# Kernel tuning notes

Hardware: AMD Instinct MI355X
Metric: run time of the kernel (lower is better)

The kernel has to match this reference:

```python
import jax, jax.numpy as jnp
import numpy as np

N_NODES = 100000
N_EDGES = 1600000
N_PAIRS = 200000
IN_C, HID_C, OUT_C = 128, 128, 64


def setup_inputs() -> dict:
    key = jax.random.key(0)
    ks = jax.random.split(key, 10)
    x = jax.random.normal(ks[0], (N_NODES, IN_C), dtype=jnp.float32)
    edge_index = jax.random.randint(ks[1], (2, N_EDGES), 0, N_NODES, dtype=jnp.int64)
    node_i = jax.random.randint(ks[2], (N_PAIRS,), 0, N_NODES, dtype=jnp.int64)
    node_j = jax.random.randint(ks[3], (N_PAIRS,), 0, N_NODES, dtype=jnp.int64)
    def glorot(k, fan_in, fan_out):
        s = jnp.sqrt(6.0 / (fan_in + fan_out))
        return jax.random.uniform(k, (fan_in, fan_out), jnp.float32, -s, s)
    W1 = glorot(ks[4], IN_C, HID_C)
    b1 = jnp.zeros((HID_C,), jnp.float32)
    W2 = glorot(ks[5], HID_C, HID_C)
    b2 = jnp.zeros((HID_C,), jnp.float32)
    W3 = glorot(ks[6], HID_C, OUT_C)
    b3 = jnp.zeros((OUT_C,), jnp.float32)
    return {"x": x, "edge_index": edge_index, "node_i": node_i, "node_j": node_j,
            "W1": W1, "b1": b1, "W2": W2, "b2": b2, "W3": W3, "b3": b3}


def _gcn_layer(h, src, dst, deg_inv, w_e, W, b):
    # h: [N, Cin] -> linear then symmetric-normalized aggregation (with self loops)
    h = h @ W  # [N, Cout]
    msg = h[src] * w_e[:, None]  # [E, Cout] gather + edge weight
    agg = jax.ops.segment_sum(msg, dst, num_segments=N_NODES)
    agg = agg + h * deg_inv[:, None]  # self-loop term: h_i / deg_i
    return agg + b


def reference(x, edge_index, node_i, node_j, W1, b1, W2, b2, W3, b3):
    src, dst = edge_index[0], edge_index[1]
    # GCN normalization with self loops: deg_i = 1 + in-degree
    ones = jnp.ones((N_EDGES,), jnp.float32)
    deg = jax.ops.segment_sum(ones, dst, num_segments=N_NODES) + 1.0
    dinv_sqrt = jax.lax.rsqrt(deg)
    deg_inv = 1.0 / deg
    w_e = dinv_sqrt[src] * dinv_sqrt[dst]  # [E]

    h = _gcn_layer(x, src, dst, deg_inv, w_e, W1, b1)
    h = jax.nn.relu(h)  # dropout is identity in eval mode
    h = _gcn_layer(h, src, dst, deg_inv, w_e, W2, b2)
    h = jax.nn.relu(h)
    h = _gcn_layer(h, src, dst, deg_inv, w_e, W3, b3)

    # dot-product link decode (decode_type=None)
    return jnp.sum(h[node_i] * h[node_j], axis=-1)  # [N_PAIRS]
```

## Files before the change

kernel.cpp:

```cpp
#include <hip/hip_runtime.h>

#define NN 100000
#define NNP 100032
#define NE 1600000
#define NP 200000
#define NBKT 782
#define BCAP 3072
#define BKB 4096

typedef short s16x8 __attribute__((ext_vector_type(8)));
typedef float f32x4 __attribute__((ext_vector_type(4)));

__device__ __forceinline__ unsigned short f2bf(float f) {
  unsigned int u = __float_as_uint(f);
  u += 0x7fffu + ((u >> 16) & 1u);
  return (unsigned short)(u >> 16);
}

__device__ __forceinline__ void upadd(uint u, float& lo, float& hi) {
  lo += __uint_as_float(u << 16);
  hi += __uint_as_float(u & 0xffff0000u);
}

template <int NT>
__device__ __forceinline__ void prepw_dev(const float* __restrict__ W,
                                          uint* __restrict__ Wt, int tid) {
  constexpr int COUT = NT * 16;
  if (tid >= 4 * NT * 64) return;
  int lane = tid & 63, comb = tid >> 6;
  int ks = comb / NT, tl = comb % NT;
  int q = lane >> 4, n = lane & 15;
  uint w[4];
#pragma unroll
  for (int jj = 0; jj < 4; ++jj) {
    int k0 = ks * 32 + q * 8 + 2 * jj;
    uint lo = f2bf(W[k0 * COUT + tl * 16 + n]);
    uint hi = f2bf(W[(k0 + 1) * COUT + tl * 16 + n]);
    w[jj] = lo | (hi << 16);
  }
  ((uint4*)Wt)[comb * 64 + lane] = make_uint4(w[0], w[1], w[2], w[3]);
}

__global__ __launch_bounds__(256) void k_setup(const float* __restrict__ W1,
                                               const float* __restrict__ W2,
                                               const float* __restrict__ W3,
                                               uint* __restrict__ Wt1,
                                               uint* __restrict__ Wt2,
                                               uint* __restrict__ Wt3,
                                               int* __restrict__ gcur) {
  int b = blockIdx.x, t = threadIdx.x;
  if (b < 4) {
    int i = b * 256 + t;
    if (i < 1024) gcur[i] = i * BCAP;
  } else if (b < 12) {
    prepw_dev<8>(W1, Wt1, (b - 4) * 256 + t);
  } else if (b < 20) {
    prepw_dev<8>(W2, Wt2, (b - 12) * 256 + t);
  } else {
    prepw_dev<4>(W3, Wt3, (b - 20) * 256 + t);
  }
}

__global__ __launch_bounds__(256) void k_bucket(const int* __restrict__ ei,
                                                int* __restrict__ gcur,
                                                int* __restrict__ aux) {
  __shared__ int cnt[1024];
  __shared__ int scn[1024];
  __shared__ int cur[1024];
  __shared__ int sc[256];
  __shared__ int sorted[BKB];
  __shared__ unsigned short sbkt[BKB];
  const int t = threadIdx.x;
  const int base = blockIdx.x * BKB;

  for (int i = t; i < 1024; i += 256) cnt[i] = 0;
  __syncthreads();

  int pk[16], bk[16];
#pragma unroll
  for (int i = 0; i < 16; ++i) {
    int e = base + t + 256 * i;
    if (e < NE) {
      int src = ei[e], dst = ei[NE + e];
      bk[i] = dst >> 7;
      pk[i] = src | ((dst & 127) << 17);
      atomicAdd(&cnt[bk[i]], 1);
    } else {
      bk[i] = -1;
    }
  }
  __syncthreads();

  int s0 = cnt[4 * t], s1 = cnt[4 * t + 1], s2 = cnt[4 * t + 2], s3 = cnt[4 * t + 3];
  int local = s0 + s1 + s2 + s3;
  sc[t] = local;
  __syncthreads();
  for (int off = 1; off < 256; off <<= 1) {
    int a = (t >= off) ? sc[t - off] : 0;
    __syncthreads();
    sc[t] += a;
    __syncthreads();
  }
  int b0 = sc[t] - local;
  scn[4 * t] = b0;
  scn[4 * t + 1] = b0 + s0;
  scn[4 * t + 2] = b0 + s0 + s1;
  scn[4 * t + 3] = b0 + s0 + s1 + s2;
  cur[4 * t] = scn[4 * t];
  cur[4 * t + 1] = scn[4 * t + 1];
  cur[4 * t + 2] = scn[4 * t + 2];
  cur[4 * t + 3] = scn[4 * t + 3];
  __syncthreads();
  const int tot = sc[255];

#pragma unroll
  for (int i = 0; i < 16; ++i) {
    if (bk[i] >= 0) {
      int pos = atomicAdd(&cur[bk[i]], 1);
      sorted[pos] = pk[i];
      sbkt[pos] = (unsigned short)bk[i];
    }
  }
  __syncthreads();

  for (int b = t; b < 1024; b += 256) {
    int c = cnt[b];
    if (c > 0) cur[b] = atomicAdd(&gcur[b], c);
  }
  __syncthreads();

  for (int k = t; k < tot; k += 256) {
    int b = sbkt[k];
    aux[cur[b] + (k - scn[b])] = sorted[k];
  }
}

__global__ __launch_bounds__(256) void k_csr(const int* __restrict__ gcur,
                                             const int* __restrict__ aux,
                                             int* __restrict__ row_ptr,
                                             float* __restrict__ dinv,
                                             int* __restrict__ col) {
  __shared__ int red[256];
  __shared__ int c[128];
  __shared__ int cur[128];
  const int b = blockIdx.x, t = threadIdx.x;
  int p = 0;
  for (int i = t; i < b; i += 256) p += gcur[i] - i * BCAP;
  red[t] = p;
  if (t < 128) c[t] = 0;
  __syncthreads();
  for (int off = 128; off > 0; off >>= 1) {
    if (t < off) red[t] += red[t + off];
    __syncthreads();
  }
  const int base = red[0];
  const int m = gcur[b] - b * BCAP;
  const int* a = aux + (size_t)b * BCAP;
  __syncthreads();
  for (int k = t; k < m; k += 256) atomicAdd(&c[a[k] >> 17], 1);
  __syncthreads();
  int val = (t < 128) ? c[t] : 0;
  red[t] = val;
  __syncthreads();
  for (int off = 1; off < 128; off <<= 1) {
    int add = (t >= off && t < 128) ? red[t - off] : 0;
    __syncthreads();
    if (t < 128) red[t] += add;
    __syncthreads();
  }
  if (t < 128) {
    int excl = red[t] - val + base;
    int node = b * 128 + t;
    if (node < NN) {
      row_ptr[node] = excl;
      dinv[node] = rsqrtf((float)(val + 1));
      cur[t] = excl;
    }
  }
  if (b == NBKT - 1 && t == 0) row_ptr[NN] = base + m;
  __syncthreads();
  for (int k = t; k < m; k += 256) {
    int pk2 = a[k];
    int pos = atomicAdd(&cur[pk2 >> 17], 1);
    col[pos] = pk2 & 0x1FFFF;
  }
}

template <int COUT, bool AFP32>
__global__ __launch_bounds__(256) void k_gemm_mfma(const void* __restrict__ Av,
                                                   const uint* __restrict__ Wt,
                                                   const float* __restrict__ dinv,
                                                   unsigned short* __restrict__ T) {
  constexpr int NT = COUT / 16;
  __shared__ __align__(16) uint Wlds[4 * NT * 64 * 4];
  __shared__ __align__(16) unsigned short Obuf[64 * COUT];
  const int t = threadIdx.x;
  {
    const uint4* src = (const uint4*)Wt;
    uint4* dst = (uint4*)Wlds;
    for (int i = t; i < 4 * NT * 64; i += 256) dst[i] = src[i];
  }
  __syncthreads();

  const int wv = t >> 6, lane = t & 63;
  const int n = lane & 15, quad = lane >> 4;
  const int rbase = blockIdx.x * 64 + wv * 16;

  union AB { uint4 u; s16x8 s; };
  AB a[4];
  if constexpr (AFP32) {
    const float* A = (const float*)Av;
    int row = rbase + n;
    if (row >= NN) row = NN - 1;
    const float* ap = A + (size_t)row * 128;
#pragma unroll
    for (int ks = 0; ks < 4; ++ks) {
      float4 v0 = *(const float4*)(ap + ks * 32 + quad * 8);
      float4 v1 = *(const float4*)(ap + ks * 32 + quad * 8 + 4);
      a[ks].u.x = (uint)f2bf(v0.x) | ((uint)f2bf(v0.y) << 16);
      a[ks].u.y = (uint)f2bf(v0.z) | ((uint)f2bf(v0.w) << 16);
      a[ks].u.z = (uint)f2bf(v1.x) | ((uint)f2bf(v1.y) << 16);
      a[ks].u.w = (uint)f2bf(v1.z) | ((uint)f2bf(v1.w) << 16);
    }
  } else {
    const uint4* A = (const uint4*)Av;
    int row = rbase + n;
#pragma unroll
    for (int ks = 0; ks < 4; ++ks) a[ks].u = A[(size_t)row * 16 + ks * 4 + quad];
  }

  f32x4 acc[NT];
#pragma unroll
  for (int tl = 0; tl < NT; ++tl) acc[tl] = (f32x4){0.f, 0.f, 0.f, 0.f};

#pragma unroll
  for (int ks = 0; ks < 4; ++ks) {
#pragma unroll
    for (int tl = 0; tl < NT; ++tl) {
      AB b;
      b.u = *(const uint4*)&Wlds[((ks * NT + tl) * 64 + lane) * 4];
      acc[tl] = __builtin_amdgcn_mfma_f32_16x16x32_bf16(a[ks].s, b.s, acc[tl], 0, 0, 0);
    }
  }

  float4 dv = *(const float4*)(dinv + rbase + quad * 4);
  float dvv[4] = {dv.x, dv.y, dv.z, dv.w};
  unsigned short* ob = Obuf + wv * 16 * COUT;
#pragma unroll
  for (int tl = 0; tl < NT; ++tl)
#pragma unroll
    for (int r = 0; r < 4; ++r)
      ob[(quad * 4 + r) * COUT + tl * 16 + n] = f2bf(acc[tl][r] * dvv[r]);

  uint4* gdst = (uint4*)(T + (size_t)rbase * COUT);
  constexpr int ITER = COUT / 32;
#pragma unroll
  for (int i = 0; i < ITER; ++i) {
    int off16 = i * 64 + lane;
    int lrow = (off16 * 8) / COUT;
    uint4 v = make_uint4(0u, 0u, 0u, 0u);
    if (rbase + lrow < NN) v = *(const uint4*)&ob[off16 * 8];
    gdst[off16] = v;
  }
}

__global__ __launch_bounds__(256) void k_gather12(const int* __restrict__ row_ptr,
                                                  const int* __restrict__ col,
                                                  const uint4* __restrict__ T4,
                                                  const float* __restrict__ dinv,
                                                  const float* __restrict__ bias,
                                                  uint4* __restrict__ An) {
  int w = (blockIdx.x * 256 + threadIdx.x) >> 6;
  int lane = threadIdx.x & 63;
  if (w >= NN) return;
  int s = row_ptr[w], tend = row_ptr[w + 1];
  const int q = lane >> 4;
  const int cl = lane & 15;
  float acc[8] = {0.f, 0.f, 0.f, 0.f, 0.f, 0.f, 0.f, 0.f};
  if (q == 0) {
    uint4 u = T4[(size_t)w * 16 + cl];
    upadd(u.x, acc[0], acc[1]);
    upadd(u.y, acc[2], acc[3]);
    upadd(u.z, acc[4], acc[5]);
    upadd(u.w, acc[6], acc[7]);
  }
  const int iters = (tend - s + 15) >> 4;
  const int m = tend - 1;
  int e = s + q;
  for (int it = 0; it < iters; ++it, e += 16) {
    int i0 = e, i1 = e + 4, i2 = e + 8, i3 = e + 12;
    int c0 = col[min(i0, m)], c1 = col[min(i1, m)];
    int c2 = col[min(i2, m)], c3 = col[min(i3, m)];
    c0 = (i0 < tend) ? c0 : NN;
    c1 = (i1 < tend) ? c1 : NN;
    c2 = (i2 < tend) ? c2 : NN;
    c3 = (i3 < tend) ? c3 : NN;
    uint4 v0 = T4[(size_t)c0 * 16 + cl];
    uint4 v1 = T4[(size_t)c1 * 16 + cl];
    uint4 v2 = T4[(size_t)c2 * 16 + cl];
    uint4 v3 = T4[(size_t)c3 * 16 + cl];
    upadd(v0.x, acc[0], acc[1]); upadd(v0.y, acc[2], acc[3]);
    upadd(v0.z, acc[4], acc[5]); upadd(v0.w, acc[6], acc[7]);
    upadd(v1.x, acc[0], acc[1]); upadd(v1.y, acc[2], acc[3]);
    upadd(v1.z, acc[4], acc[5]); upadd(v1.w, acc[6], acc[7]);
    upadd(v2.x, acc[0], acc[1]); upadd(v2.y, acc[2], acc[3]);
    upadd(v2.z, acc[4], acc[5]); upadd(v2.w, acc[6], acc[7]);
    upadd(v3.x, acc[0], acc[1]); upadd(v3.y, acc[2], acc[3]);
    upadd(v3.z, acc[4], acc[5]); upadd(v3.w, acc[6], acc[7]);
  }
#pragma unroll
  for (int i = 0; i < 8; ++i) {
    acc[i] += __shfl_down(acc[i], 16, 64);
    acc[i] += __shfl_down(acc[i], 32, 64);
  }
  if (q == 0) {
    float4 b0 = *(const float4*)&bias[cl * 8];
    float4 b1 = *(const float4*)&bias[cl * 8 + 4];
    float dv = dinv[w];
    float r[8];
    r[0] = fmaxf(fmaf(dv, acc[0], b0.x), 0.f);
    r[1] = fmaxf(fmaf(dv, acc[1], b0.y), 0.f);
    r[2] = fmaxf(fmaf(dv, acc[2], b0.z), 0.f);
    r[3] = fmaxf(fmaf(dv, acc[3], b0.w), 0.f);
    r[4] = fmaxf(fmaf(dv, acc[4], b1.x), 0.f);
    r[5] = fmaxf(fmaf(dv, acc[5], b1.y), 0.f);
    r[6] = fmaxf(fmaf(dv, acc[6], b1.z), 0.f);
    r[7] = fmaxf(fmaf(dv, acc[7], b1.w), 0.f);
    uint4 o;
    o.x = (uint)f2bf(r[0]) | ((uint)f2bf(r[1]) << 16);
    o.y = (uint)f2bf(r[2]) | ((uint)f2bf(r[3]) << 16);
    o.z = (uint)f2bf(r[4]) | ((uint)f2bf(r[5]) << 16);
    o.w = (uint)f2bf(r[6]) | ((uint)f2bf(r[7]) << 16);
    An[(size_t)w * 16 + cl] = o;
  }
}

__global__ __launch_bounds__(256) void k_gather3(const int* __restrict__ row_ptr,
                                                 const int* __restrict__ col,
                                                 const uint4* __restrict__ T4,
                                                 float* __restrict__ G3) {
  int w = (blockIdx.x * 256 + threadIdx.x) >> 6;
  int lane = threadIdx.x & 63;
  if (w >= NN) return;
  int s = row_ptr[w], tend = row_ptr[w + 1];
  const int g = lane >> 3;
  const int cl = lane & 7;
  float acc[8] = {0.f, 0.f, 0.f, 0.f, 0.f, 0.f, 0.f, 0.f};
  if (g == 0) {
    uint4 u = T4[(size_t)w * 8 + cl];
    upadd(u.x, acc[0], acc[1]);
    upadd(u.y, acc[2], acc[3]);
    upadd(u.z, acc[4], acc[5]);
    upadd(u.w, acc[6], acc[7]);
  }
  const int iters = (tend - s + 15) >> 4;
  const int m = tend - 1;
  int e = s + g;
  for (int it = 0; it < iters; ++it, e += 16) {
    int i0 = e, i1 = e + 8;
    int c0 = col[min(i0, m)], c1 = col[min(i1, m)];
    c0 = (i0 < tend) ? c0 : NN;
    c1 = (i1 < tend) ? c1 : NN;
    uint4 v0 = T4[(size_t)c0 * 8 + cl];
    uint4 v1 = T4[(size_t)c1 * 8 + cl];
    upadd(v0.x, acc[0], acc[1]); upadd(v0.y, acc[2], acc[3]);
    upadd(v0.z, acc[4], acc[5]); upadd(v0.w, acc[6], acc[7]);
    upadd(v1.x, acc[0], acc[1]); upadd(v1.y, acc[2], acc[3]);
    upadd(v1.z, acc[4], acc[5]); upadd(v1.w, acc[6], acc[7]);
  }
#pragma unroll
  for (int i = 0; i < 8; ++i) {
    acc[i] += __shfl_down(acc[i], 8, 64);
    acc[i] += __shfl_down(acc[i], 16, 64);
    acc[i] += __shfl_down(acc[i], 32, 64);
  }
  if (g == 0) {
    float* gp = &G3[(size_t)w * 64 + cl * 8];
    *(float4*)gp = make_float4(acc[0], acc[1], acc[2], acc[3]);
    *(float4*)(gp + 4) = make_float4(acc[4], acc[5], acc[6], acc[7]);
  }
}

__global__ __launch_bounds__(256) void k_decode(const int* __restrict__ ni,
                                                const int* __restrict__ nj,
                                                const float* __restrict__ G3,
                                                const float* __restrict__ dinv,
                                                const float* __restrict__ b3,
                                                float* __restrict__ out) {
  int p = blockIdx.x * 16 + (threadIdx.x >> 4);
  int cl = threadIdx.x & 15;
  int i = ni[p], j = nj[p];
  float4 gi = *(const float4*)&G3[(size_t)i * 64 + cl * 4];
  float4 gj = *(const float4*)&G3[(size_t)j * 64 + cl * 4];
  float4 bb = *(const float4*)&b3[cl * 4];
  float di = dinv[i], dj = dinv[j];
  float v = fmaf(di, gi.x, bb.x) * fmaf(dj, gj.x, bb.x) +
            fmaf(di, gi.y, bb.y) * fmaf(dj, gj.y, bb.y) +
            fmaf(di, gi.z, bb.z) * fmaf(dj, gj.z, bb.z) +
            fmaf(di, gi.w, bb.w) * fmaf(dj, gj.w, bb.w);
  v += __shfl_xor(v, 1, 64);
  v += __shfl_xor(v, 2, 64);
  v += __shfl_xor(v, 4, 64);
  v += __shfl_xor(v, 8, 64);
  if (cl == 0) out[p] = v;
}

extern "C" void kernel_launch(void* const* d_in, const int* in_sizes, int n_in,
                              void* d_out, int out_size, void* d_ws, size_t ws_size,
                              hipStream_t stream) {
  const float* x  = (const float*)d_in[0];
  const int*   ei = (const int*)d_in[1];
  const int*   ni = (const int*)d_in[2];
  const int*   nj = (const int*)d_in[3];
  const float* W1 = (const float*)d_in[4];
  const float* b1 = (const float*)d_in[5];
  const float* W2 = (const float*)d_in[6];
  const float* b2 = (const float*)d_in[7];
  const float* W3 = (const float*)d_in[8];
  const float* b3 = (const float*)d_in[9];
  float* out = (float*)d_out;

  float* dinv    = (float*)d_ws;
  int*   row_ptr = (int*)(dinv + 102400);
  int*   gcur    = row_ptr + 102400;
  int*   col     = gcur + 1024;
  uint*  Wt1     = (uint*)(col + NE);
  uint*  Wt2     = Wt1 + 8192;
  uint*  Wt3     = Wt2 + 8192;
  uint*  Tbf     = Wt3 + 4096;
  uint*  Abf     = Tbf + (size_t)NNP * 64;
  float* G3      = (float*)(Abf + (size_t)NNP * 64);
  int*   aux     = (int*)G3;

  k_setup<<<24, 256, 0, stream>>>(W1, W2, W3, Wt1, Wt2, Wt3, gcur);
  k_bucket<<<(NE + BKB - 1) / BKB, 256, 0, stream>>>(ei, gcur, aux);
  k_csr<<<NBKT, 256, 0, stream>>>(gcur, aux, row_ptr, dinv, col);

  const int GB = NNP / 64;
  const int GATB = (NN * 64 + 255) / 256;

  k_gemm_mfma<128, true><<<GB, 256, 0, stream>>>(x, Wt1, dinv, (unsigned short*)Tbf);
  k_gather12<<<GATB, 256, 0, stream>>>(row_ptr, col, (const uint4*)Tbf, dinv, b1, (uint4*)Abf);
  k_gemm_mfma<128, false><<<GB, 256, 0, stream>>>(Abf, Wt2, dinv, (unsigned short*)Tbf);
  k_gather12<<<GATB, 256, 0, stream>>>(row_ptr, col, (const uint4*)Tbf, dinv, b2, (uint4*)Abf);
  k_gemm_mfma<64, false><<<GB, 256, 0, stream>>>(Abf, Wt3, dinv, (unsigned short*)Tbf);
  k_gather3<<<GATB, 256, 0, stream>>>(row_ptr, col, (const uint4*)Tbf, G3);
  k_decode<<<NP / 16, 256, 0, stream>>>(ni, nj, G3, dinv, b3, out);
}
```

Measured before the change: 345.0 us.

## Store layer-3 aggregates in bf16, split gather loops into full and tail parts

The layer-3 gather output G3 is now written as packed bf16 instead of fp32, which halves its write traffic and the gather traffic in the decode kernel. The gather12 and gather3 loops now handle full 16-edge chunks without per-index clamps and predicates, and the masked path runs only for the remainder. The bucket counters now start at zero and the bucket base offset is added at use, which removes subtractions in the CSR kernel. Rounding G3 to bf16 adds precision loss to the final dot products.

New measurement: 339.6 us. No clear change (-1.6%).

```diff
diff --git a/kernel.cpp b/kernel.cpp
--- a/kernel.cpp
+++ b/kernel.cpp
@@ -51,7 +51,7 @@
   int b = blockIdx.x, t = threadIdx.x;
   if (b < 4) {
     int i = b * 256 + t;
-    if (i < 1024) gcur[i] = i * BCAP;
+    if (i < 1024) gcur[i] = 0;
   } else if (b < 12) {
     prepw_dev<8>(W1, Wt1, (b - 4) * 256 + t);
   } else if (b < 20) {
@@ -125,7 +125,7 @@
 
   for (int b = t; b < 1024; b += 256) {
     int c = cnt[b];
-    if (c > 0) cur[b] = atomicAdd(&gcur[b], c);
+    if (c > 0) cur[b] = b * BCAP + atomicAdd(&gcur[b], c);
   }
   __syncthreads();
 
@@ -145,7 +145,7 @@
   __shared__ int cur[128];
   const int b = blockIdx.x, t = threadIdx.x;
   int p = 0;
-  for (int i = t; i < b; i += 256) p += gcur[i] - i * BCAP;
+  for (int i = t; i < b; i += 256) p += gcur[i];
   red[t] = p;
   if (t < 128) c[t] = 0;
   __syncthreads();
@@ -154,7 +154,7 @@
     __syncthreads();
   }
   const int base = red[0];
-  const int m = gcur[b] - b * BCAP;
+  const int m = gcur[b];
   const int* a = aux + (size_t)b * BCAP;
   __syncthreads();
   for (int k = t; k < m; k += 256) atomicAdd(&c[a[k] >> 17], 1);
@@ -284,10 +284,26 @@
     upadd(u.z, acc[4], acc[5]);
     upadd(u.w, acc[6], acc[7]);
   }
-  const int iters = (tend - s + 15) >> 4;
-  const int m = tend - 1;
+  const int d = tend - s;
+  const int nfull = d >> 4;
   int e = s + q;
-  for (int it = 0; it < iters; ++it, e += 16) {
+  for (int it = 0; it < nfull; ++it, e += 16) {
+    int c0 = col[e], c1 = col[e + 4], c2 = col[e + 8], c3 = col[e + 12];
+    uint4 v0 = T4[(size_t)c0 * 16 + cl];
+    uint4 v1 = T4[(size_t)c1 * 16 + cl];
+    uint4 v2 = T4[(size_t)c2 * 16 + cl];
+    uint4 v3 = T4[(size_t)c3 * 16 + cl];
+    upadd(v0.x, acc[0], acc[1]); upadd(v0.y, acc[2], acc[3]);
+    upadd(v0.z, acc[4], acc[5]); upadd(v0.w, acc[6], acc[7]);
+    upadd(v1.x, acc[0], acc[1]); upadd(v1.y, acc[2], acc[3]);
+    upadd(v1.z, acc[4], acc[5]); upadd(v1.w, acc[6], acc[7]);
+    upadd(v2.x, acc[0], acc[1]); upadd(v2.y, acc[2], acc[3]);
+    upadd(v2.z, acc[4], acc[5]); upadd(v2.w, acc[6], acc[7]);
+    upadd(v3.x, acc[0], acc[1]); upadd(v3.y, acc[2], acc[3]);
+    upadd(v3.z, acc[4], acc[5]); upadd(v3.w, acc[6], acc[7]);
+  }
+  if (d & 15) {
+    const int m = tend - 1;
     int i0 = e, i1 = e + 4, i2 = e + 8, i3 = e + 12;
     int c0 = col[min(i0, m)], c1 = col[min(i1, m)];
     int c2 = col[min(i2, m)], c3 = col[min(i3, m)];
@@ -338,7 +354,7 @@
 __global__ __launch_bounds__(256) void k_gather3(const int* __restrict__ row_ptr,
                                                  const int* __restrict__ col,
                                                  const uint4* __restrict__ T4,
-                                                 float* __restrict__ G3) {
+                                                 uint4* __restrict__ G3) {
   int w = (blockIdx.x * 256 + threadIdx.x) >> 6;
   int lane = threadIdx.x & 63;
   if (w >= NN) return;
@@ -353,10 +369,20 @@
     upadd(u.z, acc[4], acc[5]);
     upadd(u.w, acc[6], acc[7]);
   }
-  const int iters = (tend - s + 15) >> 4;
-  const int m = tend - 1;
+  const int d = tend - s;
+  const int nfull = d >> 4;
   int e = s + g;
-  for (int it = 0; it < iters; ++it, e += 16) {
+  for (int it = 0; it < nfull; ++it, e += 16) {
+    int c0 = col[e], c1 = col[e + 8];
+    uint4 v0 = T4[(size_t)c0 * 8 + cl];
+    uint4 v1 = T4[(size_t)c1 * 8 + cl];
+    upadd(v0.x, acc[0], acc[1]); upadd(v0.y, acc[2], acc[3]);
+    upadd(v0.z, acc[4], acc[5]); upadd(v0.w, acc[6], acc[7]);
+    upadd(v1.x, acc[0], acc[1]); upadd(v1.y, acc[2], acc[3]);
+    upadd(v1.z, acc[4], acc[5]); upadd(v1.w, acc[6], acc[7]);
+  }
+  if (d & 15) {
+    const int m = tend - 1;
     int i0 = e, i1 = e + 8;
     int c0 = col[min(i0, m)], c1 = col[min(i1, m)];
     c0 = (i0 < tend) ? c0 : NN;
@@ -375,29 +401,36 @@
     acc[i] += __shfl_down(acc[i], 32, 64);
   }
   if (g == 0) {
-    float* gp = &G3[(size_t)w * 64 + cl * 8];
-    *(float4*)gp = make_float4(acc[0], acc[1], acc[2], acc[3]);
-    *(float4*)(gp + 4) = make_float4(acc[4], acc[5], acc[6], acc[7]);
+    uint4 o;
+    o.x = (uint)f2bf(acc[0]) | ((uint)f2bf(acc[1]) << 16);
+    o.y = (uint)f2bf(acc[2]) | ((uint)f2bf(acc[3]) << 16);
+    o.z = (uint)f2bf(acc[4]) | ((uint)f2bf(acc[5]) << 16);
+    o.w = (uint)f2bf(acc[6]) | ((uint)f2bf(acc[7]) << 16);
+    G3[(size_t)w * 8 + cl] = o;
   }
 }
 
 __global__ __launch_bounds__(256) void k_decode(const int* __restrict__ ni,
                                                 const int* __restrict__ nj,
-                                                const float* __restrict__ G3,
+                                                const uint2* __restrict__ G3,
                                                 const float* __restrict__ dinv,
                                                 const float* __restrict__ b3,
                                                 float* __restrict__ out) {
   int p = blockIdx.x * 16 + (threadIdx.x >> 4);
   int cl = threadIdx.x & 15;
   int i = ni[p], j = nj[p];
-  float4 gi = *(const float4*)&G3[(size_t)i * 64 + cl * 4];
-  float4 gj = *(const float4*)&G3[(size_t)j * 64 + cl * 4];
+  uint2 ui = G3[(size_t)i * 16 + cl];
+  uint2 uj = G3[(size_t)j * 16 + cl];
   float4 bb = *(const float4*)&b3[cl * 4];
   float di = dinv[i], dj = dinv[j];
-  float v = fmaf(di, gi.x, bb.x) * fmaf(dj, gj.x, bb.x) +
-            fmaf(di, gi.y, bb.y) * fmaf(dj, gj.y, bb.y) +
-            fmaf(di, gi.z, bb.z) * fmaf(dj, gj.z, bb.z) +
-            fmaf(di, gi.w, bb.w) * fmaf(dj, gj.w, bb.w);
+  float gi0 = __uint_as_float(ui.x << 16), gi1 = __uint_as_float(ui.x & 0xffff0000u);
+  float gi2 = __uint_as_float(ui.y << 16), gi3 = __uint_as_float(ui.y & 0xffff0000u);
+  float gj0 = __uint_as_float(uj.x << 16), gj1 = __uint_as_float(uj.x & 0xffff0000u);
+  float gj2 = __uint_as_float(uj.y << 16), gj3 = __uint_as_float(uj.y & 0xffff0000u);
+  float v = fmaf(di, gi0, bb.x) * fmaf(dj, gj0, bb.x) +
+            fmaf(di, gi1, bb.y) * fmaf(dj, gj1, bb.y) +
+            fmaf(di, gi2, bb.z) * fmaf(dj, gj2, bb.z) +
+            fmaf(di, gi3, bb.w) * fmaf(dj, gj3, bb.w);
   v += __shfl_xor(v, 1, 64);
   v += __shfl_xor(v, 2, 64);
   v += __shfl_xor(v, 4, 64);
@@ -429,7 +462,7 @@
   uint*  Wt3     = Wt2 + 8192;
   uint*  Tbf     = Wt3 + 4096;
   uint*  Abf     = Tbf + (size_t)NNP * 64;
-  float* G3      = (float*)(Abf + (size_t)NNP * 64);
+  uint*  G3      = Abf + (size_t)NNP * 64;
   int*   aux     = (int*)G3;
 
   k_setup<<<24, 256, 0, stream>>>(W1, W2, W3, Wt1, Wt2, Wt3, gcur);
@@ -444,6 +477,6 @@
   k_gemm_mfma<128, false><<<GB, 256, 0, stream>>>(Abf, Wt2, dinv, (unsigned short*)Tbf);
   k_gather12<<<GATB, 256, 0, stream>>>(row_ptr, col, (const uint4*)Tbf, dinv, b2, (uint4*)Abf);
   k_gemm_mfma<64, false><<<GB, 256, 0, stream>>>(Abf, Wt3, dinv, (unsigned short*)Tbf);
-  k_gather3<<<GATB, 256, 0, stream>>>(row_ptr, col, (const uint4*)Tbf, G3);
-  k_decode<<<NP / 16, 256, 0, stream>>>(ni, nj, G3, dinv, b3, out);
-}
+  k_gather3<<<GATB, 256, 0, stream>>>(row_ptr, col, (const uint4*)Tbf, (uint4*)G3);
+  k_decode<<<NP / 16, 256, 0, stream>>>(ni, nj, (const uint2*)G3, dinv, b3, out);
+}
```
